# Kernel tuning notes

Measured on AMD Instinct MI355X. Metric: run time of the kernel, lower is better.

## Reference

```python
import jax, jax.numpy as jnp
import numpy as np

B, S, D = 1, 1024, 1024
NH, NKV, HD = 16, 4, 64
E, K, HE = 64, 6, 512
EPS = 1e-5


def rmsnorm(x, w, eps=EPS):
    return w * (x * jax.lax.rsqrt(jnp.mean(x * x, axis=-1, keepdims=True) + eps))


def rope(x, cos, sin):
    # x: [b, s, h, hd]; cos/sin: [s, hd//2]; pairs are consecutive elements
    x2 = x.reshape(*x.shape[:-1], -1, 2)
    x0, x1 = x2[..., 0], x2[..., 1]
    c = cos[None, :, None, :]
    s = sin[None, :, None, :]
    o0 = x0 * c - x1 * s
    o1 = x0 * s + x1 * c
    return jnp.stack([o0, o1], axis=-1).reshape(x.shape)


def swiglu(x, w1, w3, w2):
    return (jax.nn.silu(x @ w1) * (x @ w3)) @ w2


def setup_inputs() -> dict:
    key = jax.random.key(0)
    ks = jax.random.split(key, 12)

    def w(k, shape, fan_in):
        return jax.random.normal(k, shape, jnp.float32) / np.sqrt(fan_in).astype(np.float32)

    # RoPE tables (theta = 10000), shape [S, HD//2]
    inv = 1.0 / (10000.0 ** (np.arange(0, HD, 2, dtype=np.float32) / HD))
    ang = np.arange(S, dtype=np.float32)[:, None] * inv[None, :]
    return {
        "x": jax.random.normal(ks[0], (B, S, D), jnp.float32),
        "freqs_cos": jnp.asarray(np.cos(ang), jnp.float32),
        "freqs_sin": jnp.asarray(np.sin(ang), jnp.float32),
        "attn_norm_w": jnp.ones((D,), jnp.float32),
        "ffn_norm_w": jnp.ones((D,), jnp.float32),
        "wq": w(ks[1], (D, NH * HD), D),
        "wk": w(ks[2], (D, NKV * HD), D),
        "wv": w(ks[3], (D, NKV * HD), D),
        "wo": w(ks[4], (NH * HD, D), NH * HD),
        "q_norm_w": jnp.ones((HD,), jnp.float32),
        "k_norm_w": jnp.ones((HD,), jnp.float32),
        "gate_w": w(ks[5], (D, E), D),
        "w1_e": w(ks[6], (E, D, HE), D),
        "w3_e": w(ks[7], (E, D, HE), D),
        "w2_e": w(ks[8], (E, HE, D), HE),
        "sw1": w(ks[9], (D, HE), D),
        "sw3": w(ks[10], (D, HE), D),
        "sw2": w(ks[11], (HE, D), HE),
    }


def reference(x, freqs_cos, freqs_sin, attn_norm_w, ffn_norm_w, wq, wk, wv, wo,
              q_norm_w, k_norm_w, gate_w, w1_e, w3_e, w2_e, sw1, sw3, sw2):
    b, s, d = x.shape
    # ---- attention (GQA + RoPE, causal) ----
    hx = rmsnorm(x, attn_norm_w)
    q = (hx @ wq).reshape(b, s, NH, HD)
    k = (hx @ wk).reshape(b, s, NKV, HD)
    v = (hx @ wv).reshape(b, s, NKV, HD)
    q = rmsnorm(q, q_norm_w)
    k = rmsnorm(k, k_norm_w)
    q = rope(q, freqs_cos, freqs_sin)
    k = rope(k, freqs_cos, freqs_sin)
    n_rep = NH // NKV
    k = jnp.repeat(k, n_rep, axis=2)  # [b,s,NH,HD]
    v = jnp.repeat(v, n_rep, axis=2)
    scores = jnp.einsum("bqhd,bkhd->bhqk", q, k) / jnp.float32(np.sqrt(HD))
    causal = jnp.tril(jnp.ones((s, s), bool))
    scores = jnp.where(causal[None, None], scores, jnp.finfo(scores.dtype).min)
    attn = jax.nn.softmax(scores, axis=-1)
    o = jnp.einsum("bhqk,bkhd->bqhd", attn, v).reshape(b, s, NH * HD) @ wo
    h = x + o

    # ---- MoE SwiGLU (top-k routing, renormalized) ----
    z = rmsnorm(h, ffn_norm_w).reshape(-1, d)  # [T, D]
    T = z.shape[0]
    probs = jax.nn.softmax(z @ gate_w, axis=-1)  # [T, E]
    topw, sel = jax.lax.top_k(probs, K)
    topw = topw / jnp.sum(topw, axis=-1, keepdims=True)
    # dense combine matrix C[t,e] = routing weight (0 if not selected)
    C = jnp.zeros((T, E), z.dtype).at[jnp.arange(T)[:, None], sel].add(topw)
    # expert SwiGLU, combine weights applied before the down-projection
    h1 = jnp.einsum("td,edh->teh", z, w1_e)
    h3 = jnp.einsum("td,edh->teh", z, w3_e)
    g = (jax.nn.silu(h1) * h3) * C[:, :, None]
    moe_out = jnp.einsum("teh,ehd->td", g, w2_e)
    shared = swiglu(z, sw1, sw3, sw2)
    return h + (moe_out + shared).reshape(b, s, d)
```

## Files before the change

kernel.cpp:

```cpp
#include <hip/hip_runtime.h>
#include <hip/hip_bf16.h>
#include <math.h>

#define D_MODEL 1024
#define SEQ     1024
#define NHEADS  16
#define NKVH    4
#define HDIM    64
#define NEXP    64
#define TOPK    6
#define HEXP    512
#define EPS     1e-5f
#define MAXTILES 120

typedef __attribute__((ext_vector_type(8))) short bf16x8;
typedef __attribute__((ext_vector_type(4))) float f32x4;

struct bfrag2 { bf16x8 hi, lo; };
struct f32x8r { float v[8]; };

__device__ __forceinline__ unsigned rne1(float a) {
  union { float f; unsigned u; } x; x.f = a;
  return (x.u + 0x7fffu + ((x.u >> 16) & 1u)) >> 16;
}
__device__ __forceinline__ float frombf(unsigned h) {
  union { float f; unsigned u; } x; x.u = h << 16; return x.f;
}
__device__ __forceinline__ void split_pack(float a, float b, unsigned& hi, unsigned& lo) {
  unsigned ha = rne1(a), hb = rne1(b);
  hi = ha | (hb << 16);
  lo = rne1(a - frombf(ha)) | (rne1(b - frombf(hb)) << 16);
}
__device__ __forceinline__ unsigned pk2bf(float a, float b) {
  return rne1(a) | (rne1(b) << 16);
}

__device__ __forceinline__ f32x4 mfma16(bf16x8 a, bf16x8 b, f32x4 c) {
  return __builtin_amdgcn_mfma_f32_16x16x32_bf16(a, b, c, 0, 0, 0);
}
__device__ __forceinline__ f32x4 mfma_sp(bf16x8 ah, bf16x8 al, const bfrag2& b, f32x4 c) {
  c = mfma16(ah, b.hi, c);
  c = mfma16(ah, b.lo, c);
  c = mfma16(al, b.hi, c);
  return c;
}

__device__ __forceinline__ void barrier_nv() {
  asm volatile("s_waitcnt lgkmcnt(0)" ::: "memory");
  __builtin_amdgcn_s_barrier();
}

__device__ __forceinline__ f32x8r loadraw8(const float* __restrict__ p, int ld) {
  f32x8r r;
#pragma unroll
  for (int i = 0; i < 8; i++) r.v[i] = p[(size_t)ld * i];
  return r;
}
__device__ __forceinline__ bfrag2 cvt_bf2(const f32x8r& f) {
  union { bf16x8 v; unsigned u[4]; } H, L;
  split_pack(f.v[0], f.v[1], H.u[0], L.u[0]);
  split_pack(f.v[2], f.v[3], H.u[1], L.u[1]);
  split_pack(f.v[4], f.v[5], H.u[2], L.u[2]);
  split_pack(f.v[6], f.v[7], H.u[3], L.u[3]);
  bfrag2 r; r.hi = H.v; r.lo = L.v; return r;
}
template<int RL>
__device__ __forceinline__ bf16x8 bfrag_lds(const ushort* __restrict__ B, int akb, int c) {
  union { bf16x8 v; ushort s[8]; } r;
#pragma unroll
  for (int j = 0; j < 8; j++) r.s[j] = B[(akb + j) * RL + c];
  return r.v;
}

__global__ __launch_bounds__(256) void rmsnorm_k(const float* __restrict__ x,
    const float* __restrict__ w, float* __restrict__ out, ushort* __restrict__ outb) {
  int t = blockIdx.x;
  const float4* xr = (const float4*)(x + (size_t)t * D_MODEL);
  float4 v = xr[threadIdx.x];
  float ss = v.x*v.x + v.y*v.y + v.z*v.z + v.w*v.w;
  for (int off = 32; off; off >>= 1) ss += __shfl_xor(ss, off);
  __shared__ float red[4];
  if ((threadIdx.x & 63) == 0) red[threadIdx.x >> 6] = ss;
  __syncthreads();
  float tot = red[0] + red[1] + red[2] + red[3];
  float inv = rsqrtf(tot * (1.f / D_MODEL) + EPS);
  float4 wv = ((const float4*)w)[threadIdx.x];
  float4 o;
  o.x = v.x * inv * wv.x; o.y = v.y * inv * wv.y;
  o.z = v.z * inv * wv.z; o.w = v.w * inv * wv.w;
  ((float4*)(out + (size_t)t * D_MODEL))[threadIdx.x] = o;
  if (outb) {
    uint2 b;
    b.x = pk2bf(o.x, o.y); b.y = pk2bf(o.z, o.w);
    *(uint2*)(outb + (size_t)t * D_MODEL + threadIdx.x * 4) = b;
  }
}

__global__ __launch_bounds__(256) void mfma_gemm_k(const float* __restrict__ A,
    const float* __restrict__ B, float* __restrict__ C, float* __restrict__ C2,
    const float* __restrict__ resid, int N, int K) {
  __shared__ short Ah[2][16][40];
  __shared__ short Al[2][16][40];
  int bm = blockIdx.y << 4, bn = blockIdx.x << 7;
  int tid = threadIdx.x, wv = tid >> 6, lane = tid & 63;
  int m_ = tid >> 4, k_ = (tid & 15) << 1;
  int arow = lane & 15, akb = (lane >> 4) << 3;
  int c0 = bn + wv * 32 + arow;
  const float* ar = A + (size_t)(bm + m_) * K + k_;
  {
    float2 a0 = *(const float2*)ar;
    unsigned hi, lo; split_pack(a0.x, a0.y, hi, lo);
    *(unsigned*)&Ah[0][m_][k_] = hi;
    *(unsigned*)&Al[0][m_][k_] = lo;
  }
  float2 aO = *(const float2*)(ar + 32);
  float2 aE;
  f32x8r bE0 = loadraw8(B + (size_t)akb * N + c0, N);
  f32x8r bE1 = loadraw8(B + (size_t)akb * N + c0 + 16, N);
  f32x8r bO0 = loadraw8(B + (size_t)(32 + akb) * N + c0, N);
  f32x8r bO1 = loadraw8(B + (size_t)(32 + akb) * N + c0 + 16, N);
  __syncthreads();
  f32x4 acc0 = {0.f,0.f,0.f,0.f}, acc1 = {0.f,0.f,0.f,0.f};
  for (int k0 = 0; k0 < K; k0 += 64) {
    {
      int kp = (k0 + 64 < K) ? k0 + 64 : 0;
      f32x8r n0 = loadraw8(B + (size_t)(kp + akb) * N + c0, N);
      f32x8r n1 = loadraw8(B + (size_t)(kp + akb) * N + c0 + 16, N);
      float2 an = *(const float2*)(ar + kp);
      bfrag2 f0 = cvt_bf2(bE0), f1 = cvt_bf2(bE1);
      bf16x8 ah = *(const bf16x8*)&Ah[0][arow][akb];
      bf16x8 al = *(const bf16x8*)&Al[0][arow][akb];
      acc0 = mfma_sp(ah, al, f0, acc0);
      acc1 = mfma_sp(ah, al, f1, acc1);
      unsigned hi, lo; split_pack(aO.x, aO.y, hi, lo);
      *(unsigned*)&Ah[1][m_][k_] = hi;
      *(unsigned*)&Al[1][m_][k_] = lo;
      barrier_nv();
      bE0 = n0; bE1 = n1; aE = an;
    }
    {
      int kp = (k0 + 96 < K) ? k0 + 96 : 0;
      f32x8r n0 = loadraw8(B + (size_t)(kp + akb) * N + c0, N);
      f32x8r n1 = loadraw8(B + (size_t)(kp + akb) * N + c0 + 16, N);
      float2 an = *(const float2*)(ar + kp);
      bfrag2 f0 = cvt_bf2(bO0), f1 = cvt_bf2(bO1);
      bf16x8 ah = *(const bf16x8*)&Ah[1][arow][akb];
      bf16x8 al = *(const bf16x8*)&Al[1][arow][akb];
      acc0 = mfma_sp(ah, al, f0, acc0);
      acc1 = mfma_sp(ah, al, f1, acc1);
      unsigned hi, lo; split_pack(aE.x, aE.y, hi, lo);
      *(unsigned*)&Ah[0][m_][k_] = hi;
      *(unsigned*)&Al[0][m_][k_] = lo;
      barrier_nv();
      bO0 = n0; bO1 = n1; aO = an;
    }
  }
  int r0 = (lane >> 4) << 2;
#pragma unroll
  for (int ri = 0; ri < 4; ri++) {
    int row = bm + r0 + ri;
    size_t o0 = (size_t)row * N + c0;
    float v0 = acc0[ri], v1 = acc1[ri];
    if (resid) { v0 += resid[o0]; v1 += resid[o0 + 16]; }
    C[o0] = v0; C[o0 + 16] = v1;
    if (C2) { C2[o0] = v0; C2[o0 + 16] = v1; }
  }
}

__global__ __launch_bounds__(64) void qknorm_rope_k(float* __restrict__ qb,
    float* __restrict__ kb, const float* __restrict__ qw, const float* __restrict__ kw,
    const float* __restrict__ fcos, const float* __restrict__ fsin) {
  int t = blockIdx.x, hid = blockIdx.y, lane = threadIdx.x;
  float* p; const float* w;
  if (hid < NHEADS) { p = qb + (size_t)t * (NHEADS*HDIM) + hid * HDIM; w = qw; }
  else              { p = kb + (size_t)t * (NKVH*HDIM) + (hid - NHEADS) * HDIM; w = kw; }
  float v = p[lane];
  float ss = v * v;
  for (int off = 32; off; off >>= 1) ss += __shfl_xor(ss, off);
  float vn = v * rsqrtf(ss * (1.f / HDIM) + EPS) * w[lane];
  int pi = lane >> 1;
  float c = fcos[t * (HDIM/2) + pi], s = fsin[t * (HDIM/2) + pi];
  float other = __shfl_xor(vn, 1);
  float o = (lane & 1) ? (other * s + vn * c) : (vn * c - other * s);
  p[lane] = o;
}

__global__ __launch_bounds__(128) void attn_mfma2(const float* __restrict__ qb,
    const float* __restrict__ kb, const float* __restrict__ vb, float* __restrict__ ob) {
  int h = blockIdx.y;
  int qt = (SEQ / 32 - 1) - blockIdx.x;
  int qbase = qt << 5;
  int kvh = h >> 2;
  int tid = threadIdx.x, wv = tid >> 6, lane = tid & 63;
  __shared__ short Kt[64][72];
  __shared__ short Vt[64][72];
  __shared__ short Pl[2][16][72];
  int arow = lane & 15;
  int akb = (lane >> 4) << 3;
  int kg = lane >> 4;
  int qrow_base = qbase + wv * 16;
  bf16x8 qf[2];
  {
    const float* qp = qb + (size_t)(qrow_base + arow) * (NHEADS*HDIM) + h * HDIM;
#pragma unroll
    for (int c = 0; c < 2; c++) {
      int d0 = akb + c * 32;
      union { bf16x8 v; unsigned u[4]; } r;
#pragma unroll
      for (int j = 0; j < 4; j++) r.u[j] = pk2bf(qp[d0 + 2*j], qp[d0 + 2*j + 1]);
      qf[c] = r.v;
    }
  }
  f32x4 accO[4];
  float m_[4], l_[4];
#pragma unroll
  for (int n = 0; n < 4; n++) { accO[n] = (f32x4){0.f,0.f,0.f,0.f}; m_[n] = -1e30f; l_[n] = 0.f; }
  int ntiles = (qbase >> 6) + 1;
  for (int ti = 0; ti < ntiles; ti++) {
    int ts = ti << 6;
#pragma unroll
    for (int i = 0; i < 8; i++) {
      int f = tid + i * 128;
      int kk = f >> 4, d4 = (f & 15) << 2;
      size_t src = (size_t)(ts + kk) * (NKVH*HDIM) + kvh * HDIM + d4;
      float4 k4 = *(const float4*)(kb + src);
      float4 v4 = *(const float4*)(vb + src);
      ushort kp0 = rne1(k4.x), kp1 = rne1(k4.y), kp2 = rne1(k4.z), kp3 = rne1(k4.w);
      unsigned* kd = (unsigned*)&Kt[kk][d4];
      kd[0] = (unsigned)kp0 | ((unsigned)kp1 << 16);
      kd[1] = (unsigned)kp2 | ((unsigned)kp3 << 16);
      Vt[d4 + 0][kk] = (short)rne1(v4.x);
      Vt[d4 + 1][kk] = (short)rne1(v4.y);
      Vt[d4 + 2][kk] = (short)rne1(v4.z);
      Vt[d4 + 3][kk] = (short)rne1(v4.w);
    }
    __syncthreads();
    f32x4 accS[4];
#pragma unroll
    for (int n = 0; n < 4; n++) accS[n] = (f32x4){0.f,0.f,0.f,0.f};
#pragma unroll
    for (int c = 0; c < 2; c++) {
#pragma unroll
      for (int n = 0; n < 4; n++) {
        bf16x8 bf = *(const bf16x8*)&Kt[n*16 + arow][c*32 + akb];
        accS[n] = mfma16(qf[c], bf, accS[n]);
      }
    }
#pragma unroll
    for (int ri = 0; ri < 4; ri++) {
      int qrow = qrow_base + kg*4 + ri;
      float mx = -1e30f;
#pragma unroll
      for (int n = 0; n < 4; n++) {
        int key = ts + n*16 + arow;
        float s = (key <= qrow) ? accS[n][ri] * 0.125f : -1e30f;
        accS[n][ri] = s;
        mx = fmaxf(mx, s);
      }
      for (int off = 1; off < 16; off <<= 1) mx = fmaxf(mx, __shfl_xor(mx, off));
      float mn = fmaxf(m_[ri], mx);
      float a = __expf(m_[ri] - mn);
      float sum = 0.f;
#pragma unroll
      for (int n = 0; n < 4; n++) {
        float p = __expf(accS[n][ri] - mn);
        accS[n][ri] = p;
        sum += p;
      }
      for (int off = 1; off < 16; off <<= 1) sum += __shfl_xor(sum, off);
      l_[ri] = l_[ri] * a + sum;
      m_[ri] = mn;
#pragma unroll
      for (int n = 0; n < 4; n++) accO[n][ri] *= a;
    }
#pragma unroll
    for (int ri = 0; ri < 4; ri++)
#pragma unroll
      for (int n = 0; n < 4; n++)
        Pl[wv][kg*4 + ri][n*16 + arow] = (short)rne1(accS[n][ri]);
#pragma unroll
    for (int c = 0; c < 2; c++) {
      bf16x8 pf = *(const bf16x8*)&Pl[wv][arow][c*32 + akb];
#pragma unroll
      for (int n = 0; n < 4; n++) {
        bf16x8 vf = *(const bf16x8*)&Vt[n*16 + arow][c*32 + akb];
        accO[n] = mfma16(pf, vf, accO[n]);
      }
    }
    __syncthreads();
  }
#pragma unroll
  for (int ri = 0; ri < 4; ri++) {
    int qrow = qrow_base + kg*4 + ri;
    float inv = 1.f / l_[ri];
#pragma unroll
    for (int n = 0; n < 4; n++)
      ob[(size_t)qrow * (NHEADS*HDIM) + h * HDIM + n*16 + arow] = accO[n][ri] * inv;
  }
}

__global__ __launch_bounds__(64) void gate_topk_k(const float* __restrict__ z,
    const float* __restrict__ gw, int* __restrict__ sel, float* __restrict__ topw,
    int* __restrict__ counts) {
  int t = blockIdx.x, lane = threadIdx.x;
  const float* zr = z + (size_t)t * D_MODEL;
  float acc = 0.f;
  for (int d = 0; d < D_MODEL; d += 4) {
    float4 zv = *(const float4*)(zr + d);
    acc += zv.x * gw[(size_t)(d + 0) * NEXP + lane];
    acc += zv.y * gw[(size_t)(d + 1) * NEXP + lane];
    acc += zv.z * gw[(size_t)(d + 2) * NEXP + lane];
    acc += zv.w * gw[(size_t)(d + 3) * NEXP + lane];
  }
  float m = acc;
  for (int off = 32; off; off >>= 1) m = fmaxf(m, __shfl_xor(m, off));
  float p = __expf(acc - m);
  float s = p;
  for (int off = 32; off; off >>= 1) s += __shfl_xor(s, off);
  p /= s;
  float rem = p, wsum = 0.f;
  float wvv[TOPK]; int wi[TOPK];
  for (int i = 0; i < TOPK; i++) {
    float v = rem; int idx = lane;
    for (int off = 32; off; off >>= 1) {
      float v2 = __shfl_xor(v, off);
      int i2 = __shfl_xor(idx, off);
      if (v2 > v || (v2 == v && i2 < idx)) { v = v2; idx = i2; }
    }
    wvv[i] = v; wi[i] = idx; wsum += v;
    if (lane == idx) rem = -1.f;
  }
  if (lane < TOPK) {
    sel[t * TOPK + lane] = wi[lane];
    topw[t * TOPK + lane] = wvv[lane] / wsum;
  }
  if (lane == 0)
    for (int i = 0; i < TOPK; i++) atomicAdd(&counts[wi[i]], 1);
}

__global__ void scan_k(const int* __restrict__ counts, int* __restrict__ offs,
                       int* __restrict__ cursor, int* __restrict__ tile2e,
                       int* __restrict__ tile2mt, int* __restrict__ ntiles) {
  int lane = threadIdx.x;
  int c = counts[lane];
  int x = c;
  for (int off = 1; off < 64; off <<= 1) {
    int y = __shfl_up(x, off);
    if (lane >= off) x += y;
  }
  offs[lane] = x - c;
  cursor[lane] = x - c;
  int nt = (c + 127) >> 7;
  int y = nt;
  for (int off = 1; off < 64; off <<= 1) {
    int t2 = __shfl_up(y, off);
    if (lane >= off) y += t2;
  }
  int tbase = y - nt;
  for (int i = 0; i < nt; i++) { tile2e[tbase + i] = lane; tile2mt[tbase + i] = i; }
  if (lane == 63) {
    for (int i = 0; i < 8; i++) { tile2e[y + i] = NEXP; tile2mt[y + i] = i; }
    ntiles[0] = y + 8;
  }
}

__global__ void scatter_k(const int* __restrict__ sel, const float* __restrict__ topw,
    int* __restrict__ cursor, int* __restrict__ tok, float* __restrict__ wt) {
  int t = blockIdx.x * 256 + threadIdx.x;
  if (t >= SEQ) return;
  for (int i = 0; i < TOPK; i++) {
    int e = sel[t * TOPK + i];
    int pos = atomicAdd(&cursor[e], 1);
    tok[pos] = t;
    wt[pos] = topw[t * TOPK + i];
  }
}

__global__ __launch_bounds__(256) void moe_up6(const ushort* __restrict__ zb,
    const float* __restrict__ w1, const float* __restrict__ w3, size_t wstride,
    const float* __restrict__ sw1, const float* __restrict__ sw3,
    ushort* __restrict__ g, ushort* __restrict__ sg,
    const int* __restrict__ tok_list, const float* __restrict__ wt_list,
    const int* __restrict__ counts, const int* __restrict__ offs,
    const int* __restrict__ tile2e, const int* __restrict__ tile2mt,
    const int* __restrict__ ntiles) {
  int gt = blockIdx.y;
  if (gt >= ntiles[0]) return;
  int e = tile2e[gt];
  int mt = tile2mt[gt] << 7;
  bool sh = (e == NEXP);
  int cnt = sh ? SEQ : counts[e];
  int off = sh ? 0 : offs[e];
  const float* w1p = (sh ? sw1 : w1 + (size_t)e * wstride) + (blockIdx.x << 6);
  const float* w3p = (sh ? sw3 : w3 + (size_t)e * wstride) + (blockIdx.x << 6);
  ushort* gout = sh ? sg : g;
  __shared__ ushort Ah[2][128][40];
  __shared__ ushort Bs[2][2][32][74];
  __shared__ int toks[128];
  int tid = threadIdx.x, wv = tid >> 6, lane = tid & 63;
  int arow = lane & 15, akb = (lane >> 4) << 3, kg = lane >> 4;
  int c0l = wv * 16 + arow;
  int c0 = (blockIdx.x << 6) + c0l;
  if (tid < 128) {
    int r = mt + tid; if (r >= cnt) r = cnt - 1;
    toks[tid] = sh ? r : tok_list[off + r];
  }
  __syncthreads();
  int row0 = tid >> 2, q8 = (tid & 3) << 3, row1 = row0 + 64;
  const ushort* zr0 = zb + (size_t)toks[row0] * D_MODEL + q8;
  const ushort* zr1 = zb + (size_t)toks[row1] * D_MODEL + q8;
  int kB = tid >> 4, cB = (tid & 15) << 2;
  const float* w1q = w1p + (size_t)kB * HEXP + cB;
  const float* w3q = w3p + (size_t)kB * HEXP + cB;
  uint4  ra0 = *(const uint4*)zr0;
  uint4  ra1 = *(const uint4*)zr1;
  float4 rb1a = *(const float4*)w1q;
  float4 rb1b = *(const float4*)(w1q + 16 * HEXP);
  float4 rb3a = *(const float4*)w3q;
  float4 rb3b = *(const float4*)(w3q + 16 * HEXP);
  f32x4 a1[8], a3[8];
#pragma unroll
  for (int f = 0; f < 8; f++) { a1[f] = (f32x4){0.f,0.f,0.f,0.f}; a3[f] = (f32x4){0.f,0.f,0.f,0.f}; }
  int cur = 0;
  for (int k0 = 0; k0 < D_MODEL; k0 += 32) {
    int kp = (k0 + 32 < D_MODEL) ? k0 + 32 : 0;
    uint4  na0 = *(const uint4*)(zr0 + kp);
    uint4  na1 = *(const uint4*)(zr1 + kp);
    const float* w1n = w1q + (size_t)kp * HEXP;
    const float* w3n = w3q + (size_t)kp * HEXP;
    float4 nb1a = *(const float4*)w1n;
    float4 nb1b = *(const float4*)(w1n + 16 * HEXP);
    float4 nb3a = *(const float4*)w3n;
    float4 nb3b = *(const float4*)(w3n + 16 * HEXP);
    *(uint4*)&Ah[cur][row0][q8] = ra0;
    *(uint4*)&Ah[cur][row1][q8] = ra1;
    {
      unsigned* p = (unsigned*)&Bs[cur][0][kB][cB];
      p[0] = pk2bf(rb1a.x, rb1a.y); p[1] = pk2bf(rb1a.z, rb1a.w);
      unsigned* p2 = (unsigned*)&Bs[cur][0][kB + 16][cB];
      p2[0] = pk2bf(rb1b.x, rb1b.y); p2[1] = pk2bf(rb1b.z, rb1b.w);
      unsigned* p3 = (unsigned*)&Bs[cur][1][kB][cB];
      p3[0] = pk2bf(rb3a.x, rb3a.y); p3[1] = pk2bf(rb3a.z, rb3a.w);
      unsigned* p4 = (unsigned*)&Bs[cur][1][kB + 16][cB];
      p4[0] = pk2bf(rb3b.x, rb3b.y); p4[1] = pk2bf(rb3b.z, rb3b.w);
    }
    barrier_nv();
    bf16x8 f1 = bfrag_lds<74>(&Bs[cur][0][0][0], akb, c0l);
    bf16x8 f3 = bfrag_lds<74>(&Bs[cur][1][0][0], akb, c0l);
#pragma unroll
    for (int f = 0; f < 8; f++) {
      bf16x8 ah = *(const bf16x8*)&Ah[cur][f*16 + arow][akb];
      a1[f] = mfma16(ah, f1, a1[f]);
      a3[f] = mfma16(ah, f3, a3[f]);
    }
    ra0 = na0; ra1 = na1;
    rb1a = nb1a; rb1b = nb1b; rb3a = nb3a; rb3b = nb3b;
    cur ^= 1;
  }
#pragma unroll
  for (int f = 0; f < 8; f++)
#pragma unroll
    for (int ri = 0; ri < 4; ri++) {
      int r = mt + f*16 + kg*4 + ri;
      if (r < cnt) {
        float wt = sh ? 1.0f : wt_list[off + r];
        float h1 = a1[f][ri], h3 = a3[f][ri];
        float gv = h1 / (1.f + __expf(-h1)) * h3 * wt;
        gout[(size_t)(off + r) * HEXP + c0] = (ushort)rne1(gv);
      }
    }
}

__global__ __launch_bounds__(256) void moe_down6(const ushort* __restrict__ g,
    const ushort* __restrict__ sg, const float* __restrict__ w2, size_t wstride,
    const float* __restrict__ sw2, float* __restrict__ out,
    const int* __restrict__ tok_list, const int* __restrict__ counts,
    const int* __restrict__ offs, const int* __restrict__ tile2e,
    const int* __restrict__ tile2mt, const int* __restrict__ ntiles) {
  int gt = blockIdx.y;
  if (gt >= ntiles[0]) return;
  int e = tile2e[gt];
  int mt = tile2mt[gt] << 7;
  bool sh = (e == NEXP);
  int cnt = sh ? SEQ : counts[e];
  int off = sh ? 0 : offs[e];
  const float* w2p = (sh ? sw2 : w2 + (size_t)e * wstride) + (blockIdx.x << 7);
  const ushort* gin = sh ? sg : g;
  __shared__ ushort Ah[2][128][40];
  __shared__ ushort Bs[2][32][138];
  int tid = threadIdx.x, wv = tid >> 6, lane = tid & 63;
  int arow = lane & 15, akb = (lane >> 4) << 3, kg = lane >> 4;
  int c0l = wv * 32 + arow;
  int c0 = (blockIdx.x << 7) + c0l;
  int row0 = tid >> 2, q8 = (tid & 3) << 3, row1 = row0 + 64;
  int rr0 = mt + row0; if (rr0 >= cnt) rr0 = cnt - 1;
  int rr1 = mt + row1; if (rr1 >= cnt) rr1 = cnt - 1;
  const ushort* gr0 = gin + (size_t)(off + rr0) * HEXP + q8;
  const ushort* gr1 = gin + (size_t)(off + rr1) * HEXP + q8;
  int kB = tid >> 3, cB = (tid & 7) << 4;
  const float* w2q = w2p + (size_t)kB * D_MODEL + cB;
  uint4  ra0 = *(const uint4*)gr0;
  uint4  ra1 = *(const uint4*)gr1;
  float4 rb0 = *(const float4*)(w2q);
  float4 rb1 = *(const float4*)(w2q + 4);
  float4 rb2 = *(const float4*)(w2q + 8);
  float4 rb3 = *(const float4*)(w2q + 12);
  f32x4 ac0[8], ac1[8];
#pragma unroll
  for (int f = 0; f < 8; f++) { ac0[f] = (f32x4){0.f,0.f,0.f,0.f}; ac1[f] = (f32x4){0.f,0.f,0.f,0.f}; }
  int cur = 0;
  for (int k0 = 0; k0 < HEXP; k0 += 32) {
    int kp = (k0 + 32 < HEXP) ? k0 + 32 : 0;
    uint4  na0 = *(const uint4*)(gr0 + kp);
    uint4  na1 = *(const uint4*)(gr1 + kp);
    const float* wn = w2q + (size_t)kp * D_MODEL;
    float4 nb0 = *(const float4*)(wn);
    float4 nb1 = *(const float4*)(wn + 4);
    float4 nb2 = *(const float4*)(wn + 8);
    float4 nb3 = *(const float4*)(wn + 12);
    *(uint4*)&Ah[cur][row0][q8] = ra0;
    *(uint4*)&Ah[cur][row1][q8] = ra1;
    {
      unsigned* p = (unsigned*)&Bs[cur][kB][cB];
      p[0] = pk2bf(rb0.x, rb0.y); p[1] = pk2bf(rb0.z, rb0.w);
      p[2] = pk2bf(rb1.x, rb1.y); p[3] = pk2bf(rb1.z, rb1.w);
      p[4] = pk2bf(rb2.x, rb2.y); p[5] = pk2bf(rb2.z, rb2.w);
      p[6] = pk2bf(rb3.x, rb3.y); p[7] = pk2bf(rb3.z, rb3.w);
    }
    barrier_nv();
    bf16x8 f0 = bfrag_lds<138>(&Bs[cur][0][0], akb, c0l);
    bf16x8 f1 = bfrag_lds<138>(&Bs[cur][0][0], akb, c0l + 16);
#pragma unroll
    for (int f = 0; f < 8; f++) {
      bf16x8 ah = *(const bf16x8*)&Ah[cur][f*16 + arow][akb];
      ac0[f] = mfma16(ah, f0, ac0[f]);
      ac1[f] = mfma16(ah, f1, ac1[f]);
    }
    ra0 = na0; ra1 = na1;
    rb0 = nb0; rb1 = nb1; rb2 = nb2; rb3 = nb3;
    cur ^= 1;
  }
#pragma unroll
  for (int f = 0; f < 8; f++)
#pragma unroll
    for (int ri = 0; ri < 4; ri++) {
      int r = mt + f*16 + kg*4 + ri;
      if (r < cnt) {
        int tok = sh ? r : tok_list[off + r];
        float* op = out + (size_t)tok * D_MODEL + c0;
        atomicAdd(op, ac0[f][ri]);
        atomicAdd(op + 16, ac1[f][ri]);
      }
    }
}

extern "C" void kernel_launch(void* const* d_in, const int* in_sizes, int n_in,
                              void* d_out, int out_size, void* d_ws, size_t ws_size,
                              hipStream_t stream) {
  const float* x     = (const float*)d_in[0];
  const float* fcos  = (const float*)d_in[1];
  const float* fsin  = (const float*)d_in[2];
  const float* anw   = (const float*)d_in[3];
  const float* fnw   = (const float*)d_in[4];
  const float* wq    = (const float*)d_in[5];
  const float* wk    = (const float*)d_in[6];
  const float* wvv   = (const float*)d_in[7];
  const float* wo    = (const float*)d_in[8];
  const float* qnw   = (const float*)d_in[9];
  const float* knw   = (const float*)d_in[10];
  const float* gatew = (const float*)d_in[11];
  const float* w1e   = (const float*)d_in[12];
  const float* w3e   = (const float*)d_in[13];
  const float* w2e   = (const float*)d_in[14];
  const float* sw1   = (const float*)d_in[15];
  const float* sw3   = (const float*)d_in[16];
  const float* sw2   = (const float*)d_in[17];
  float* out = (float*)d_out;

  char* ws = (char*)d_ws;
  const size_t MB = 1ull << 20;
  float*  hx    = (float*)(ws);
  float*  h     = (float*)(ws + 4*MB);
  float*  z     = (float*)(ws + 8*MB);
  float*  qbuf  = (float*)(ws + 12*MB);
  float*  kbuf  = (float*)(ws + 16*MB);
  float*  vbuf  = (float*)(ws + 17*MB);
  ushort* zb    = (ushort*)(ws + 12*MB);
  ushort* gb    = (ushort*)(ws + 14*MB);
  ushort* s_gb  = (ushort*)(ws + 20*MB + 512*1024);
  char*   misc  = ws + 22*MB;
  int*   sel      = (int*)(misc);
  float* topw     = (float*)(misc + 24576);
  int*   counts   = (int*)(misc + 49152);
  int*   offs     = (int*)(misc + 49408);
  int*   cursor   = (int*)(misc + 49664);
  int*   ntiles   = (int*)(misc + 50432);
  int*   tile2e   = (int*)(misc + 50688);
  int*   tile2mt  = (int*)(misc + 51200);
  int*   tok_list = (int*)(misc + 51712);
  float* wt_list  = (float*)(misc + 76288);

  rmsnorm_k<<<SEQ, 256, 0, stream>>>(x, anw, hx, nullptr);
  mfma_gemm_k<<<dim3(8, 64), 256, 0, stream>>>(hx, wq, qbuf, nullptr, nullptr, 1024, 1024);
  mfma_gemm_k<<<dim3(2, 64), 256, 0, stream>>>(hx, wk, kbuf, nullptr, nullptr, 256, 1024);
  mfma_gemm_k<<<dim3(2, 64), 256, 0, stream>>>(hx, wvv, vbuf, nullptr, nullptr, 256, 1024);
  qknorm_rope_k<<<dim3(SEQ, NHEADS + NKVH), 64, 0, stream>>>(qbuf, kbuf, qnw, knw, fcos, fsin);
  attn_mfma2<<<dim3(SEQ / 32, NHEADS), 128, 0, stream>>>(qbuf, kbuf, vbuf, hx);
  mfma_gemm_k<<<dim3(8, 64), 256, 0, stream>>>(hx, wo, h, out, x, 1024, 1024);
  rmsnorm_k<<<SEQ, 256, 0, stream>>>(h, fnw, z, zb);
  hipMemsetAsync(counts, 0, 256, stream);
  gate_topk_k<<<SEQ, 64, 0, stream>>>(z, gatew, sel, topw, counts);
  scan_k<<<1, 64, 0, stream>>>(counts, offs, cursor, tile2e, tile2mt, ntiles);
  scatter_k<<<SEQ / 256, 256, 0, stream>>>(sel, topw, cursor, tok_list, wt_list);
  moe_up6<<<dim3(HEXP / 64, MAXTILES), 256, 0, stream>>>(zb, w1e, w3e,
      (size_t)D_MODEL * HEXP, sw1, sw3, gb, s_gb, tok_list, wt_list,
      counts, offs, tile2e, tile2mt, ntiles);
  moe_down6<<<dim3(D_MODEL / 128, MAXTILES), 256, 0, stream>>>(gb, s_gb, w2e,
      (size_t)HEXP * D_MODEL, sw2, out, tok_list, counts, offs,
      tile2e, tile2mt, ntiles);
  (void)in_sizes; (void)n_in; (void)out_size; (void)ws_size;
}
```

Before: 419.5 us.

## Fuse QKV projections into one single-bf16 GEMM and widen attention tiles

Merges the three Q/K/V projection launches into one kernel that picks its weight matrix from the block index. That kernel uses plain bf16 instead of the hi/lo split bf16 emulation, which halves the MFMA work and LDS traffic but lowers precision of the projections. The attention kernel moves from 32-query blocks with 2 waves to 64-query blocks with 4 waves, so each K/V tile load serves more queries. Larger attention blocks halve the block count and may worsen causal load balance.

```diff
diff --git a/kernel.cpp b/kernel.cpp
--- a/kernel.cpp
+++ b/kernel.cpp
@@ -63,6 +63,12 @@
   split_pack(f.v[4], f.v[5], H.u[2], L.u[2]);
   split_pack(f.v[6], f.v[7], H.u[3], L.u[3]);
   bfrag2 r; r.hi = H.v; r.lo = L.v; return r;
+}
+__device__ __forceinline__ bf16x8 cvt_bf(const f32x8r& f) {
+  union { bf16x8 v; unsigned u[4]; } r;
+  r.u[0] = pk2bf(f.v[0], f.v[1]); r.u[1] = pk2bf(f.v[2], f.v[3]);
+  r.u[2] = pk2bf(f.v[4], f.v[5]); r.u[3] = pk2bf(f.v[6], f.v[7]);
+  return r.v;
 }
 template<int RL>
 __device__ __forceinline__ bf16x8 bfrag_lds(const ushort* __restrict__ B, int akb, int c) {
@@ -93,6 +99,72 @@
     uint2 b;
     b.x = pk2bf(o.x, o.y); b.y = pk2bf(o.z, o.w);
     *(uint2*)(outb + (size_t)t * D_MODEL + threadIdx.x * 4) = b;
+  }
+}
+
+__global__ __launch_bounds__(256) void mfma_gemm_qkv(const float* __restrict__ A,
+    const float* __restrict__ WQ, const float* __restrict__ WK,
+    const float* __restrict__ WV, float* __restrict__ Q, float* __restrict__ Kb,
+    float* __restrict__ V) {
+  const float* B; float* C; int N, bn;
+  int bx = blockIdx.x;
+  if (bx < 8)       { B = WQ; C = Q;  N = 1024; bn = bx << 7; }
+  else if (bx < 10) { B = WK; C = Kb; N = 256;  bn = (bx - 8) << 7; }
+  else              { B = WV; C = V;  N = 256;  bn = (bx - 10) << 7; }
+  const int K = 1024;
+  __shared__ short Ah[2][16][40];
+  int bm = blockIdx.y << 4;
+  int tid = threadIdx.x, wv = tid >> 6, lane = tid & 63;
+  int m_ = tid >> 4, k_ = (tid & 15) << 1;
+  int arow = lane & 15, akb = (lane >> 4) << 3;
+  int c0 = bn + wv * 32 + arow;
+  const float* ar = A + (size_t)(bm + m_) * K + k_;
+  {
+    float2 a0 = *(const float2*)ar;
+    *(unsigned*)&Ah[0][m_][k_] = pk2bf(a0.x, a0.y);
+  }
+  float2 aO = *(const float2*)(ar + 32);
+  float2 aE;
+  f32x8r bE0 = loadraw8(B + (size_t)akb * N + c0, N);
+  f32x8r bE1 = loadraw8(B + (size_t)akb * N + c0 + 16, N);
+  f32x8r bO0 = loadraw8(B + (size_t)(32 + akb) * N + c0, N);
+  f32x8r bO1 = loadraw8(B + (size_t)(32 + akb) * N + c0 + 16, N);
+  __syncthreads();
+  f32x4 acc0 = {0.f,0.f,0.f,0.f}, acc1 = {0.f,0.f,0.f,0.f};
+  for (int k0 = 0; k0 < K; k0 += 64) {
+    {
+      int kp = (k0 + 64 < K) ? k0 + 64 : 0;
+      f32x8r n0 = loadraw8(B + (size_t)(kp + akb) * N + c0, N);
+      f32x8r n1 = loadraw8(B + (size_t)(kp + akb) * N + c0 + 16, N);
+      float2 an = *(const float2*)(ar + kp);
+      bf16x8 f0 = cvt_bf(bE0), f1 = cvt_bf(bE1);
+      bf16x8 ah = *(const bf16x8*)&Ah[0][arow][akb];
+      acc0 = mfma16(ah, f0, acc0);
+      acc1 = mfma16(ah, f1, acc1);
+      *(unsigned*)&Ah[1][m_][k_] = pk2bf(aO.x, aO.y);
+      barrier_nv();
+      bE0 = n0; bE1 = n1; aE = an;
+    }
+    {
+      int kp = (k0 + 96 < K) ? k0 + 96 : 0;
+      f32x8r n0 = loadraw8(B + (size_t)(kp + akb) * N + c0, N);
+      f32x8r n1 = loadraw8(B + (size_t)(kp + akb) * N + c0 + 16, N);
+      float2 an = *(const float2*)(ar + kp);
+      bf16x8 f0 = cvt_bf(bO0), f1 = cvt_bf(bO1);
+      bf16x8 ah = *(const bf16x8*)&Ah[1][arow][akb];
+      acc0 = mfma16(ah, f0, acc0);
+      acc1 = mfma16(ah, f1, acc1);
+      *(unsigned*)&Ah[0][m_][k_] = pk2bf(aE.x, aE.y);
+      barrier_nv();
+      bO0 = n0; bO1 = n1; aO = an;
+    }
+  }
+  int r0 = (lane >> 4) << 2;
+#pragma unroll
+  for (int ri = 0; ri < 4; ri++) {
+    size_t o0 = (size_t)(bm + r0 + ri) * N + c0;
+    C[o0] = acc0[ri];
+    C[o0 + 16] = acc1[ri];
   }
 }
 
@@ -185,16 +257,15 @@
   p[lane] = o;
 }
 
-__global__ __launch_bounds__(128) void attn_mfma2(const float* __restrict__ qb,
+__global__ __launch_bounds__(256) void attn_mfma(const float* __restrict__ qb,
     const float* __restrict__ kb, const float* __restrict__ vb, float* __restrict__ ob) {
   int h = blockIdx.y;
-  int qt = (SEQ / 32 - 1) - blockIdx.x;
-  int qbase = qt << 5;
+  int qbase = ((SEQ / 64 - 1) - blockIdx.x) << 6;
   int kvh = h >> 2;
   int tid = threadIdx.x, wv = tid >> 6, lane = tid & 63;
   __shared__ short Kt[64][72];
   __shared__ short Vt[64][72];
-  __shared__ short Pl[2][16][72];
+  __shared__ short Pl[4][16][72];
   int arow = lane & 15;
   int akb = (lane >> 4) << 3;
   int kg = lane >> 4;
@@ -219,16 +290,15 @@
   for (int ti = 0; ti < ntiles; ti++) {
     int ts = ti << 6;
 #pragma unroll
-    for (int i = 0; i < 8; i++) {
-      int f = tid + i * 128;
+    for (int i = 0; i < 4; i++) {
+      int f = tid + i * 256;
       int kk = f >> 4, d4 = (f & 15) << 2;
       size_t src = (size_t)(ts + kk) * (NKVH*HDIM) + kvh * HDIM + d4;
       float4 k4 = *(const float4*)(kb + src);
       float4 v4 = *(const float4*)(vb + src);
-      ushort kp0 = rne1(k4.x), kp1 = rne1(k4.y), kp2 = rne1(k4.z), kp3 = rne1(k4.w);
       unsigned* kd = (unsigned*)&Kt[kk][d4];
-      kd[0] = (unsigned)kp0 | ((unsigned)kp1 << 16);
-      kd[1] = (unsigned)kp2 | ((unsigned)kp3 << 16);
+      kd[0] = pk2bf(k4.x, k4.y);
+      kd[1] = pk2bf(k4.z, k4.w);
       Vt[d4 + 0][kk] = (short)rne1(v4.x);
       Vt[d4 + 1][kk] = (short)rne1(v4.y);
       Vt[d4 + 2][kk] = (short)rne1(v4.z);
@@ -601,11 +671,9 @@
   float* wt_list  = (float*)(misc + 76288);
 
   rmsnorm_k<<<SEQ, 256, 0, stream>>>(x, anw, hx, nullptr);
-  mfma_gemm_k<<<dim3(8, 64), 256, 0, stream>>>(hx, wq, qbuf, nullptr, nullptr, 1024, 1024);
-  mfma_gemm_k<<<dim3(2, 64), 256, 0, stream>>>(hx, wk, kbuf, nullptr, nullptr, 256, 1024);
-  mfma_gemm_k<<<dim3(2, 64), 256, 0, stream>>>(hx, wvv, vbuf, nullptr, nullptr, 256, 1024);
+  mfma_gemm_qkv<<<dim3(12, 64), 256, 0, stream>>>(hx, wq, wk, wvv, qbuf, kbuf, vbuf);
   qknorm_rope_k<<<dim3(SEQ, NHEADS + NKVH), 64, 0, stream>>>(qbuf, kbuf, qnw, knw, fcos, fsin);
-  attn_mfma2<<<dim3(SEQ / 32, NHEADS), 128, 0, stream>>>(qbuf, kbuf, vbuf, hx);
+  attn_mfma<<<dim3(SEQ / 64, NHEADS), 256, 0, stream>>>(qbuf, kbuf, vbuf, hx);
   mfma_gemm_k<<<dim3(8, 64), 256, 0, stream>>>(hx, wo, h, out, x, 1024, 1024);
   rmsnorm_k<<<SEQ, 256, 0, stream>>>(h, fnw, z, zb);
   hipMemsetAsync(counts, 0, 256, stream);
```

Result: faster. 340.2 us (-18.9%).
